# Performance work log

Hardware: AMD Instinct MI355X
Metric: run time of the kernel (lower is better)

The kernel has to match this reference:

```python
import jax, jax.numpy as jnp
import numpy as np

Ng, Np, T, B = 2048, 512, 100, 256


def setup_inputs() -> dict:
    key = jax.random.key(0)
    ks = jax.random.split(key, 16)
    s = lambda fan_in: 1.0 / np.sqrt(fan_in)
    return {
        "v": jax.random.normal(ks[0], (B, T, 2), jnp.float32),
        "p0": jax.random.uniform(ks[1], (B, Np), jnp.float32),
        "enc1_W": jax.random.normal(ks[2], (Np, Ng), jnp.float32) * s(Np),
        "enc1_b": jnp.zeros((Ng,), jnp.float32),
        "enc2_W": jax.random.normal(ks[3], (Np, Ng), jnp.float32) * s(Np),
        "enc2_b": jnp.zeros((Ng,), jnp.float32),
        "M_W": jax.random.normal(ks[4], (2, Ng), jnp.float32) * s(2),
        "M_b": jnp.zeros((Ng,), jnp.float32),
        "lstm_W": jax.random.normal(ks[5], (Ng, 4 * Ng), jnp.float32) * s(Ng),
        "lstm_U": jax.random.normal(ks[6], (Ng, 4 * Ng), jnp.float32) * s(Ng),
        "lstm_b": jnp.zeros((4 * Ng,), jnp.float32),
        "dense_W": jax.random.normal(ks[7], (Ng, Ng), jnp.float32) * s(Ng),
        "dense_b": jnp.zeros((Ng,), jnp.float32),
        "dec_W": jax.random.normal(ks[8], (Ng, Np), jnp.float32) * s(Ng),
        "dec_b": jnp.zeros((Np,), jnp.float32),
    }


def reference(v, p0, enc1_W, enc1_b, enc2_W, enc2_b, M_W, M_b,
              lstm_W, lstm_U, lstm_b, dense_W, dense_b, dec_W, dec_b):
    # initial LSTM state from place-cell code: (h0, c0)
    h0 = p0 @ enc1_W + enc1_b                      # [B, Ng]
    c0 = p0 @ enc2_W + enc2_b                      # [B, Ng]
    Mv = v @ M_W + M_b                             # [B, T, Ng]
    # precompute input-to-gate projections for all timesteps
    x_gates = Mv @ lstm_W + lstm_b                 # [B, T, 4*Ng]

    def step(carry, xt):
        h, c = carry
        z = xt + h @ lstm_U                        # [B, 4*Ng]
        i, f, g, o = jnp.split(z, 4, axis=-1)      # Keras gate order i,f,c,o
        i = jax.nn.sigmoid(i)
        f = jax.nn.sigmoid(f)
        g = jax.nn.relu(g)                         # activation='relu'
        o = jax.nn.sigmoid(o)
        c = f * c + i * g
        h = o * jax.nn.relu(c)
        return (h, c), h

    xs = jnp.swapaxes(x_gates, 0, 1)               # [T, B, 4*Ng]
    _, hs = jax.lax.scan(step, (h0, c0), xs)       # hs: [T, B, Ng]
    rnn = jnp.swapaxes(hs, 0, 1)                   # [B, T, Ng]
    g_cells = jax.nn.relu(rnn @ dense_W + dense_b) # [B, T, Ng]
    place_preds = g_cells @ dec_W + dec_b          # [B, T, Np]
    return place_preds
```

## Files before the change

### kernel.cpp

```cpp
#include <hip/hip_runtime.h>
#include <stdint.h>

#define DI __device__ __forceinline__

typedef short s16x8 __attribute__((ext_vector_type(8)));
typedef float f32x4 __attribute__((ext_vector_type(4)));

#define NG   2048
#define NP   512
#define TT   100
#define BB   256
#define N4   8192
#define MR   25600
#define NBLK 256

DI unsigned short f32_to_bf16(float f) {
  union { float f; uint32_t u; } x; x.f = f;
  uint32_t r = x.u + 0x7fffu + ((x.u >> 16) & 1u);
  return (unsigned short)(r >> 16);
}

DI void async16(const void* g, void* l) {
  __builtin_amdgcn_global_load_lds((const __attribute__((address_space(1))) void*)g,
                                   (__attribute__((address_space(3))) void*)l,
                                   16, 0, 0);
}

DI f32x4 mfma16(s16x8 a, s16x8 b, f32x4 c) {
  return __builtin_amdgcn_mfma_f32_16x16x32_bf16(a, b, c, 0, 0, 0);
}

__global__ __launch_bounds__(256) void k_zero(unsigned* p) {
  if (threadIdx.x < 160) p[threadIdx.x] = 0u;
}

DI void grid_barrier2(unsigned* bar, int xcd, int t) {
  asm volatile("s_waitcnt vmcnt(0)" ::: "memory");
  __syncthreads();
  if (threadIdx.x == 0) {
    unsigned a = __hip_atomic_fetch_add(bar + xcd * 16, 1u,
                                        __ATOMIC_RELAXED, __HIP_MEMORY_SCOPE_AGENT);
    if (a + 1u == 32u * (unsigned)(t + 1)) {
      unsigned g2 = __hip_atomic_fetch_add(bar + 128, 1u,
                                           __ATOMIC_RELAXED, __HIP_MEMORY_SCOPE_AGENT);
      if (g2 + 1u == 8u * (unsigned)(t + 1))
        __hip_atomic_store(bar + 144, (unsigned)(t + 1),
                           __ATOMIC_RELAXED, __HIP_MEMORY_SCOPE_AGENT);
    }
    while (__hip_atomic_load(bar + 144, __ATOMIC_RELAXED,
                             __HIP_MEMORY_SCOPE_AGENT) < (unsigned)(t + 1))
      __builtin_amdgcn_s_sleep(8);
  }
  __syncthreads();
}

template <int BM>
DI void gemm_core_p(const unsigned short* __restrict__ A, int lda, int m0,
                    const unsigned short* __restrict__ Bt, int ldb, int n0, int K,
                    unsigned short* sA, unsigned short* sB, f32x4* acc) {
  constexpr int FM = BM / 32;
  const int tid  = threadIdx.x;
  const int wave = tid >> 6;
  const int lane = tid & 63;
  const int quad = lane >> 4;
  const int lr   = lane & 15;
  const int wm   = wave >> 2;
  const int wn   = wave & 3;
  const int lr8  = lane >> 3;
  const int lc8  = lane & 7;
  const int scol = (lc8 ^ lr8) << 3;

  const int nkt = K >> 6;
  int buf = 0;

  auto stage = [&](int bsel, int k0) {
    unsigned short* dA = sA + bsel * (BM * 64);
    unsigned short* dB = sB + bsel * (128 * 64);
#pragma unroll
    for (int c = 0; c < BM / 64; ++c) {
      int rbase = wave * (BM / 8) + c * 8;
      const unsigned short* g = A + (size_t)(m0 + rbase + lr8) * lda + (k0 + scol);
      async16(g, dA + rbase * 64);
    }
#pragma unroll
    for (int c = 0; c < 2; ++c) {
      int rbase = wave * 16 + c * 8;
      const unsigned short* g = Bt + (size_t)(n0 + rbase + lr8) * ldb + (k0 + scol);
      async16(g, dB + rbase * 64);
    }
  };

  stage(0, 0);
  __syncthreads();
  for (int kt = 0; kt < nkt; ++kt) {
    if (kt + 1 < nkt) stage(buf ^ 1, (kt + 1) << 6);
    const char* cA = (const char*)(sA + buf * (BM * 64));
    const char* cB = (const char*)(sB + buf * (128 * 64));
#pragma unroll
    for (int ks = 0; ks < 2; ++ks) {
      s16x8 af[FM], bfr[2];
#pragma unroll
      for (int fm = 0; fm < FM; ++fm) {
        int row = wm * (BM / 2) + fm * 16 + lr;
        int off = row * 128 + ((ks * 64 + quad * 16) ^ ((row & 7) << 4));
        af[fm] = *(const s16x8*)(cA + off);
      }
#pragma unroll
      for (int fn = 0; fn < 2; ++fn) {
        int col = wn * 32 + fn * 16 + lr;
        int off = col * 128 + ((ks * 64 + quad * 16) ^ ((col & 7) << 4));
        bfr[fn] = *(const s16x8*)(cB + off);
      }
#pragma unroll
      for (int fm = 0; fm < FM; ++fm)
#pragma unroll
        for (int fn = 0; fn < 2; ++fn)
          acc[fm * 2 + fn] = mfma16(af[fm], bfr[fn], acc[fm * 2 + fn]);
    }
    __syncthreads();
    buf ^= 1;
  }
}

template <int MODE>
__global__ __launch_bounds__(256) void k_transpose_bf16(
    const float* __restrict__ src, unsigned short* __restrict__ dst,
    int R, int C, int noff) {
  __shared__ unsigned short tile[64][65];
  int tr0 = blockIdx.x * 64;
  int tc0 = blockIdx.y * 64;
  int tid = threadIdx.x;
#pragma unroll
  for (int i = 0; i < 16; ++i) {
    int idx = tid + i * 256;
    int r = idx >> 6, c = idx & 63;
    tile[r][c] = f32_to_bf16(src[(size_t)(tr0 + r) * C + (tc0 + c)]);
  }
  __syncthreads();
#pragma unroll
  for (int i = 0; i < 16; ++i) {
    int idx = tid + i * 256;
    int cc = idx >> 6, r = idx & 63;
    int c = tc0 + cc;
    int n = (MODE == 0) ? (c + noff) : (((c & 2047) << 2) | (c >> 11));
    dst[(size_t)n * R + (tr0 + r)] = tile[r][cc];
  }
}

__global__ __launch_bounds__(256) void k_cvt(const float* __restrict__ src,
                                             unsigned short* __restrict__ dst, int n) {
  int i = blockIdx.x * 256 + threadIdx.x;
  if (i < n) dst[i] = f32_to_bf16(src[i]);
}

__global__ __launch_bounds__(256) void k_prep_xw_part(
    const float* __restrict__ lstm_W, const float* __restrict__ M_W,
    const float* __restrict__ M_b, float* __restrict__ part) {
  int c = blockIdx.x * 256 + threadIdx.x;
  int kc = blockIdx.y;
  int k0 = kc * 128;
  float a0 = 0.f, a1 = 0.f, ab = 0.f;
  for (int k = k0; k < k0 + 128; ++k) {
    float w = lstm_W[(size_t)k * N4 + c];
    a0 += M_W[k] * w;
    a1 += M_W[NG + k] * w;
    ab += M_b[k] * w;
  }
  float* p = part + (size_t)kc * 3 * N4;
  p[c] = a0; p[N4 + c] = a1; p[2 * N4 + c] = ab;
}

__global__ __launch_bounds__(256) void k_prep_xw_reduce(
    const float* __restrict__ part, const float* __restrict__ lstm_b,
    float* __restrict__ W2r, float* __restrict__ b2r) {
  int c = blockIdx.x * 256 + threadIdx.x;
  float a0 = 0.f, a1 = 0.f, ab = 0.f;
  for (int kc = 0; kc < 16; ++kc) {
    const float* p = part + (size_t)kc * 3 * N4;
    a0 += p[c]; a1 += p[N4 + c]; ab += p[2 * N4 + c];
  }
  int n = ((c & 2047) << 2) | (c >> 11);
  W2r[n] = a0; W2r[N4 + n] = a1; b2r[n] = ab + lstm_b[c];
}

__global__ __launch_bounds__(512) void k_enc(
    const unsigned short* __restrict__ p0b, const unsigned short* __restrict__ encWt,
    const float* __restrict__ enc1_b, const float* __restrict__ enc2_b,
    unsigned short* __restrict__ hbf, float* __restrict__ cfp) {
  __shared__ __align__(16) unsigned short sA[2 * 64 * 64];
  __shared__ __align__(16) unsigned short sB[2 * 128 * 64];
  int m0 = blockIdx.x * 64, n0 = blockIdx.y * 128;
  const f32x4 vzero = {0.f, 0.f, 0.f, 0.f};
  f32x4 acc[4];
#pragma unroll
  for (int i = 0; i < 4; ++i) acc[i] = vzero;
  gemm_core_p<64>(p0b, NP, m0, encWt, NP, n0, NP, sA, sB, acc);

  const int tid = threadIdx.x, wave = tid >> 6, lane = tid & 63;
  const int quad = lane >> 4, lr = lane & 15, wm = wave >> 2, wn = wave & 3;
#pragma unroll
  for (int fm = 0; fm < 2; ++fm)
#pragma unroll
    for (int fn = 0; fn < 2; ++fn)
#pragma unroll
      for (int reg = 0; reg < 4; ++reg) {
        int grow = m0 + wm * 32 + fm * 16 + quad * 4 + reg;
        int gcol = n0 + wn * 32 + fn * 16 + lr;
        float val = acc[fm * 2 + fn][reg];
        if (gcol < NG)
          hbf[(size_t)grow * NG + gcol] = f32_to_bf16(val + enc1_b[gcol]);
        else
          cfp[(size_t)grow * NG + (gcol - NG)] = val + enc2_b[gcol - NG];
      }
}

__global__ __launch_bounds__(512) void k_steps(
    const unsigned short* __restrict__ Ut,
    const float* __restrict__ vv, const float* __restrict__ W2r,
    const float* __restrict__ b2r, float* __restrict__ cfp,
    const unsigned short* __restrict__ hb0,
    unsigned short* __restrict__ hs, unsigned* __restrict__ bar) {
  __shared__ __align__(16) char smem[98304];

  const int bid = blockIdx.x;
  const int xcd = bid & 7, sb = bid >> 3;
  const int mt = sb >> 3, nsub = sb & 7;
  const int nt = xcd * 8 + nsub;
  const int m0 = mt * 64, n0 = nt * 128;
  const int tid = threadIdx.x;
  const int wave = tid >> 6, lane = tid & 63;
  const int quad = lane >> 4, lr = lane & 15, wm = wave >> 2, wn = wave & 3;
  const int lr8 = lane >> 3, lc8 = lane & 7;
  const int scol = (lc8 ^ lr8) << 3;

  const int j = tid & 31;
  const int gbase = n0 + 4 * j;
  const float4 w2a   = *(const float4*)(W2r + gbase);
  const float4 w2b   = *(const float4*)(W2r + N4 + gbase);
  const float4 bbias = *(const float4*)(b2r + gbase);
  const int cell = (n0 >> 2) + j;
  const int r0 = tid >> 5;

  asm volatile("s_waitcnt vmcnt(0)" ::: "memory");

  for (int t = 0; t < TT; ++t) {
    const unsigned short* hin = (t == 0) ? hb0 : (hs + (size_t)(t - 1) * BB * NG);

    const f32x4 vzero = {0.f, 0.f, 0.f, 0.f};
    f32x4 acc[4];
#pragma unroll
    for (int i = 0; i < 4; ++i) acc[i] = vzero;

    auto stageS = [&](int kt) {
      const int slot = kt & 3;
      const int k0 = kt << 6;
      {
        const int rbase = wave * 8;
        const unsigned short* g = hin + (size_t)(m0 + rbase + lr8) * NG + (k0 + scol);
        async16(g, smem + slot * 8192 + rbase * 128);
      }
#pragma unroll
      for (int c = 0; c < 2; ++c) {
        const int rbase = wave * 16 + c * 8;
        const unsigned short* g = Ut + (size_t)(n0 + rbase + lr8) * NG + (k0 + scol);
        async16(g, smem + 32768 + slot * 16384 + rbase * 128);
      }
    };
    auto computeS = [&](int kt) {
      const char* cA = smem + (kt & 3) * 8192;
      const char* cB = smem + 32768 + (kt & 3) * 16384;
#pragma unroll
      for (int ks = 0; ks < 2; ++ks) {
        s16x8 af[2], bfr[2];
#pragma unroll
        for (int fm = 0; fm < 2; ++fm) {
          const int row = wm * 32 + fm * 16 + lr;
          af[fm] = *(const s16x8*)(cA + row * 128 + ((ks * 64 + quad * 16) ^ ((row & 7) << 4)));
        }
#pragma unroll
        for (int fn = 0; fn < 2; ++fn) {
          const int col = wn * 32 + fn * 16 + lr;
          bfr[fn] = *(const s16x8*)(cB + col * 128 + ((ks * 64 + quad * 16) ^ ((col & 7) << 4)));
        }
#pragma unroll
        for (int fm = 0; fm < 2; ++fm)
#pragma unroll
          for (int fn = 0; fn < 2; ++fn)
            acc[fm * 2 + fn] = mfma16(af[fm], bfr[fn], acc[fm * 2 + fn]);
      }
    };

    stageS(0); stageS(1); stageS(2);
    for (int kt = 0; kt < 29; ++kt) {
      asm volatile("s_barrier" ::: "memory");
      stageS(kt + 3);
      asm volatile("s_waitcnt vmcnt(9)\n\ts_barrier" ::: "memory");
      computeS(kt);
    }
    asm volatile("s_waitcnt vmcnt(6)\n\ts_barrier" ::: "memory");
    computeS(29);
    asm volatile("s_waitcnt vmcnt(3)\n\ts_barrier" ::: "memory");
    computeS(30);
    asm volatile("s_waitcnt vmcnt(0)\n\ts_barrier" ::: "memory");
    computeS(31);
    __syncthreads();

    float* zs = (float*)smem;
#pragma unroll
    for (int fm = 0; fm < 2; ++fm)
#pragma unroll
      for (int fn = 0; fn < 2; ++fn)
#pragma unroll
        for (int reg = 0; reg < 4; ++reg) {
          const int r  = wm * 32 + fm * 16 + quad * 4 + reg;
          const int cc = wn * 32 + fn * 16 + lr;
          zs[r * 132 + cc] = acc[fm * 2 + fn][reg];
        }
    __syncthreads();
    unsigned short* htmp = (unsigned short*)(smem + 33792);
#pragma unroll
    for (int i = 0; i < 4; ++i) {
      const int r = r0 + i * 16;
      const int b = m0 + r;
      const float2 vb = *(const float2*)(vv + ((size_t)b * TT + t) * 2);
      float4 z4 = *(const float4*)(zs + r * 132 + 4 * j);
      float zi = z4.x + vb.x * w2a.x + vb.y * w2b.x + bbias.x;
      float zf = z4.y + vb.x * w2a.y + vb.y * w2b.y + bbias.y;
      float zg = z4.z + vb.x * w2a.z + vb.y * w2b.z + bbias.z;
      float zo = z4.w + vb.x * w2a.w + vb.y * w2b.w + bbias.w;
      float i_ = 1.f / (1.f + __expf(-zi));
      float f_ = 1.f / (1.f + __expf(-zf));
      float g_ = fmaxf(zg, 0.f);
      float o_ = 1.f / (1.f + __expf(-zo));
      const size_t ci = (size_t)b * NG + cell;
      float cn = f_ * cfp[ci] + i_ * g_;
      cfp[ci] = cn;
      htmp[r * 32 + j] = f32_to_bf16(o_ * fmaxf(cn, 0.f));
    }
    __syncthreads();
    const unsigned* hw = (const unsigned*)htmp;
#pragma unroll
    for (int p = 0; p < 2; ++p) {
      const int q = tid + p * 512;
      const int r = q >> 4, cq = q & 15;
      unsigned* hp = (unsigned*)(hs + ((size_t)t * BB + m0 + r) * NG + (n0 >> 2)) + cq;
      __hip_atomic_store(hp, hw[q], __ATOMIC_RELAXED, __HIP_MEMORY_SCOPE_AGENT);
    }
    if (t + 1 < TT) grid_barrier2(bar, xcd, t);
  }
}

__global__ __launch_bounds__(512) void k_dense(
    const unsigned short* __restrict__ hs, const unsigned short* __restrict__ dWt,
    const float* __restrict__ dense_b, unsigned short* __restrict__ gc) {
  __shared__ __align__(16) unsigned short sA[2 * 128 * 64];
  __shared__ __align__(16) unsigned short sB[2 * 128 * 64];
  int bid = blockIdx.x;
  int mt = bid >> 4;
  int r4 = bid & 15;
  int nt = ((r4 & 7) << 1) | (r4 >> 3);
  int m0 = mt * 128, n0 = nt * 128;
  const f32x4 vzero = {0.f, 0.f, 0.f, 0.f};
  f32x4 acc[8];
#pragma unroll
  for (int i = 0; i < 8; ++i) acc[i] = vzero;
  gemm_core_p<128>(hs, NG, m0, dWt, NG, n0, NG, sA, sB, acc);

  const int tid = threadIdx.x, wave = tid >> 6, lane = tid & 63;
  const int quad = lane >> 4, lr = lane & 15, wm = wave >> 2, wn = wave & 3;
#pragma unroll
  for (int fm = 0; fm < 4; ++fm)
#pragma unroll
    for (int fn = 0; fn < 2; ++fn)
#pragma unroll
      for (int reg = 0; reg < 4; ++reg) {
        int grow = m0 + wm * 64 + fm * 16 + quad * 4 + reg;
        int gcol = n0 + wn * 32 + fn * 16 + lr;
        float val = fmaxf(acc[fm * 2 + fn][reg] + dense_b[gcol], 0.f);
        gc[(size_t)grow * NG + gcol] = f32_to_bf16(val);
      }
}

__global__ __launch_bounds__(512) void k_dec(
    const unsigned short* __restrict__ gc, const unsigned short* __restrict__ decWt,
    const float* __restrict__ dec_b, float* __restrict__ out) {
  __shared__ __align__(16) unsigned short sA[2 * 128 * 64];
  __shared__ __align__(16) unsigned short sB[2 * 128 * 64];
  int m0 = blockIdx.x * 128, n0 = blockIdx.y * 128;
  const f32x4 vzero = {0.f, 0.f, 0.f, 0.f};
  f32x4 acc[8];
#pragma unroll
  for (int i = 0; i < 8; ++i) acc[i] = vzero;
  gemm_core_p<128>(gc, NG, m0, decWt, NG, n0, NG, sA, sB, acc);

  const int tid = threadIdx.x, wave = tid >> 6, lane = tid & 63;
  const int quad = lane >> 4, lr = lane & 15, wm = wave >> 2, wn = wave & 3;
#pragma unroll
  for (int fm = 0; fm < 4; ++fm)
#pragma unroll
    for (int fn = 0; fn < 2; ++fn)
#pragma unroll
      for (int reg = 0; reg < 4; ++reg) {
        int grow = m0 + wm * 64 + fm * 16 + quad * 4 + reg;
        int gcol = n0 + wn * 32 + fn * 16 + lr;
        int tt = grow >> 8, b = grow & 255;
        out[((size_t)b * TT + tt) * NP + gcol] = acc[fm * 2 + fn][reg] + dec_b[gcol];
      }
}

extern "C" void kernel_launch(void* const* d_in, const int* in_sizes, int n_in,
                              void* d_out, int out_size, void* d_ws, size_t ws_size,
                              hipStream_t stream) {
  (void)in_sizes; (void)n_in; (void)out_size; (void)ws_size;
  const float* v       = (const float*)d_in[0];
  const float* p0      = (const float*)d_in[1];
  const float* enc1_W  = (const float*)d_in[2];
  const float* enc1_b  = (const float*)d_in[3];
  const float* enc2_W  = (const float*)d_in[4];
  const float* enc2_b  = (const float*)d_in[5];
  const float* M_W     = (const float*)d_in[6];
  const float* M_b     = (const float*)d_in[7];
  const float* lstm_W  = (const float*)d_in[8];
  const float* lstm_U  = (const float*)d_in[9];
  const float* lstm_b  = (const float*)d_in[10];
  const float* dense_W = (const float*)d_in[11];
  const float* dense_b = (const float*)d_in[12];
  const float* dec_W   = (const float*)d_in[13];
  const float* dec_b   = (const float*)d_in[14];
  float* out = (float*)d_out;

  char* ws = (char*)d_ws;
  size_t off = 0;
  auto alloc = [&](size_t bytes) {
    char* p = ws + off;
    off += (bytes + 255) & ~(size_t)255;
    return p;
  };
  unsigned short* Ut    = (unsigned short*)alloc((size_t)N4 * NG * 2);
  unsigned short* dWt   = (unsigned short*)alloc((size_t)NG * NG * 2);
  unsigned short* decWt = (unsigned short*)alloc((size_t)NP * NG * 2);
  unsigned short* encWt = (unsigned short*)alloc((size_t)2 * NG * NP * 2);
  unsigned short* p0b   = (unsigned short*)alloc((size_t)BB * NP * 2);
  float* W2r  = (float*)alloc((size_t)2 * N4 * 4);
  float* b2r  = (float*)alloc((size_t)N4 * 4);
  float* part = (float*)alloc((size_t)16 * 3 * N4 * 4);
  float* cfp  = (float*)alloc((size_t)BB * NG * 4);
  unsigned short* hb0 = (unsigned short*)alloc((size_t)BB * NG * 2);
  unsigned short* hs  = (unsigned short*)alloc((size_t)MR * NG * 2);
  unsigned short* gc  = (unsigned short*)alloc((size_t)MR * NG * 2);
  unsigned* bar = (unsigned*)alloc(1024);

  dim3 blk(256), blk5(512);
  k_zero<<<dim3(1), blk, 0, stream>>>(bar);
  k_transpose_bf16<1><<<dim3(32, 128), blk, 0, stream>>>(lstm_U, Ut, NG, N4, 0);
  k_transpose_bf16<0><<<dim3(32, 32), blk, 0, stream>>>(dense_W, dWt, NG, NG, 0);
  k_transpose_bf16<0><<<dim3(32, 8), blk, 0, stream>>>(dec_W, decWt, NG, NP, 0);
  k_transpose_bf16<0><<<dim3(8, 32), blk, 0, stream>>>(enc1_W, encWt, NP, NG, 0);
  k_transpose_bf16<0><<<dim3(8, 32), blk, 0, stream>>>(enc2_W, encWt, NP, NG, NG);
  k_cvt<<<dim3(512), blk, 0, stream>>>(p0, p0b, BB * NP);
  k_prep_xw_part<<<dim3(32, 16), blk, 0, stream>>>(lstm_W, M_W, M_b, part);
  k_prep_xw_reduce<<<dim3(32), blk, 0, stream>>>(part, lstm_b, W2r, b2r);
  k_enc<<<dim3(4, 32), blk5, 0, stream>>>(p0b, encWt, enc1_b, enc2_b, hb0, cfp);
  k_steps<<<dim3(NBLK), blk5, 0, stream>>>(Ut, v, W2r, b2r, cfp, hb0, hs, bar);
  k_dense<<<dim3(3200), blk5, 0, stream>>>(hs, dWt, dense_b, gc);
  k_dec<<<dim3(200, 4), blk5, 0, stream>>>(gc, decWt, dec_b, out);
}
```

Before: 2.135 ms.

## Restructure LSTM step kernel: register-resident cell state, gate-grouped layout, cross-step pipeline

The persistent recurrent kernel now uses 256 threads per block, each wave computing a 32x64 tile. The U-transpose and bias/weight permutations are rearranged so that the i/f/g/o gates for one cell fall in the same lane across four accumulator fragments, which lets the gate math run straight from MFMA accumulators without going through a shared-memory staging tile. Cell state stays in registers for all timesteps instead of being read and written in global memory each step. A 5-slot ring buffer prefetches the first U tiles of the next timestep before the grid barrier, and v values are loaded asynchronously into LDS. The cost is heavier register pressure and more complex wait-count bookkeeping.

Result: faster. 2.091 ms (-2.0%).

```diff
diff --git a/kernel.cpp b/kernel.cpp
--- a/kernel.cpp
+++ b/kernel.cpp
@@ -24,6 +24,11 @@
   __builtin_amdgcn_global_load_lds((const __attribute__((address_space(1))) void*)g,
                                    (__attribute__((address_space(3))) void*)l,
                                    16, 0, 0);
+}
+DI void async4(const void* g, void* l) {
+  __builtin_amdgcn_global_load_lds((const __attribute__((address_space(1))) void*)g,
+                                   (__attribute__((address_space(3))) void*)l,
+                                   4, 0, 0);
 }
 
 DI f32x4 mfma16(s16x8 a, s16x8 b, f32x4 c) {
@@ -142,7 +147,8 @@
     int idx = tid + i * 256;
     int cc = idx >> 6, r = idx & 63;
     int c = tc0 + cc;
-    int n = (MODE == 0) ? (c + noff) : (((c & 2047) << 2) | (c >> 11));
+    int n = (MODE == 0) ? (c + noff)
+                        : ((((c & 2047) >> 4) << 6) | (((c >> 11) & 3) << 4) | (c & 15));
     dst[(size_t)n * R + (tr0 + r)] = tile[r][cc];
   }
 }
@@ -179,7 +185,7 @@
     const float* p = part + (size_t)kc * 3 * N4;
     a0 += p[c]; a1 += p[N4 + c]; ab += p[2 * N4 + c];
   }
-  int n = ((c & 2047) << 2) | (c >> 11);
+  int n = (((c & 2047) >> 4) << 6) | (((c >> 11) & 3) << 4) | (c & 15);
   W2r[n] = a0; W2r[N4 + n] = a1; b2r[n] = ab + lstm_b[c];
 }
 
@@ -214,13 +220,13 @@
       }
 }
 
-__global__ __launch_bounds__(512) void k_steps(
+__global__ __launch_bounds__(256) void k_steps(
     const unsigned short* __restrict__ Ut,
     const float* __restrict__ vv, const float* __restrict__ W2r,
-    const float* __restrict__ b2r, float* __restrict__ cfp,
+    const float* __restrict__ b2r, const float* __restrict__ cfp,
     const unsigned short* __restrict__ hb0,
     unsigned short* __restrict__ hs, unsigned* __restrict__ bar) {
-  __shared__ __align__(16) char smem[98304];
+  __shared__ __align__(16) char smem[127488];
 
   const int bid = blockIdx.x;
   const int xcd = bid & 7, sb = bid >> 3;
@@ -229,125 +235,149 @@
   const int m0 = mt * 64, n0 = nt * 128;
   const int tid = threadIdx.x;
   const int wave = tid >> 6, lane = tid & 63;
-  const int quad = lane >> 4, lr = lane & 15, wm = wave >> 2, wn = wave & 3;
+  const int quad = lane >> 4, lr = lane & 15;
+  const int wm = wave >> 1, wn = wave & 1;
   const int lr8 = lane >> 3, lc8 = lane & 7;
   const int scol = (lc8 ^ lr8) << 3;
 
-  const int j = tid & 31;
-  const int gbase = n0 + 4 * j;
-  const float4 w2a   = *(const float4*)(W2r + gbase);
-  const float4 w2b   = *(const float4*)(W2r + N4 + gbase);
-  const float4 bbias = *(const float4*)(b2r + gbase);
-  const int cell = (n0 >> 2) + j;
-  const int r0 = tid >> 5;
+  float w2x[4], w2y[4], bz[4];
+#pragma unroll
+  for (int g = 0; g < 4; ++g) {
+    const int idx = n0 + wn * 64 + g * 16 + lr;
+    w2x[g] = W2r[idx]; w2y[g] = W2r[N4 + idx]; bz[g] = b2r[idx];
+    asm volatile("" : "+v"(w2x[g])); asm volatile("" : "+v"(w2y[g]));
+    asm volatile("" : "+v"(bz[g]));
+  }
+  const int cellg = nt * 32 + wn * 16 + lr;
+  float cst[2][4];
+#pragma unroll
+  for (int fm = 0; fm < 2; ++fm)
+#pragma unroll
+    for (int reg = 0; reg < 4; ++reg) {
+      const int r = wm * 32 + fm * 16 + quad * 4 + reg;
+      cst[fm][reg] = cfp[(size_t)(m0 + r) * NG + cellg];
+      asm volatile("" : "+v"(cst[fm][reg]));
+    }
+
+  auto stageA = [&](int slot, int kt, const unsigned short* hin) {
+#pragma unroll
+    for (int c = 0; c < 2; ++c) {
+      const int rb = wave * 16 + c * 8;
+      const unsigned short* g = hin + (size_t)(m0 + rb + lr8) * NG + ((kt << 6) + scol);
+      async16(g, smem + slot * 8192 + rb * 128);
+    }
+  };
+  auto stageB = [&](int slot, int k) {
+#pragma unroll
+    for (int c = 0; c < 4; ++c) {
+      const int rb = wave * 32 + c * 8;
+      const unsigned short* g = Ut + (size_t)(n0 + rb + lr8) * NG + (k + scol);
+      async16(g, smem + 40960 + slot * 16384 + rb * 128);
+    }
+  };
+  auto stageV = [&](int t) {
+    const float* gx = vv + ((size_t)(m0 + lane) * TT + t) * 2;
+    async4(gx, smem + 122880);
+    async4(gx + 1, smem + 123136);
+  };
+
+  f32x4 acc[8];
+  auto computeS = [&](int slot) {
+    const char* cA = smem + slot * 8192;
+    const char* cB = smem + 40960 + slot * 16384;
+#pragma unroll
+    for (int ks = 0; ks < 2; ++ks) {
+      s16x8 af[2], bfr[4];
+#pragma unroll
+      for (int fm = 0; fm < 2; ++fm) {
+        const int row = wm * 32 + fm * 16 + lr;
+        af[fm] = *(const s16x8*)(cA + row * 128 + ((ks * 64 + quad * 16) ^ ((row & 7) << 4)));
+      }
+#pragma unroll
+      for (int fn = 0; fn < 4; ++fn) {
+        const int col = wn * 64 + fn * 16 + lr;
+        bfr[fn] = *(const s16x8*)(cB + col * 128 + ((ks * 64 + quad * 16) ^ ((col & 7) << 4)));
+      }
+#pragma unroll
+      for (int fm = 0; fm < 2; ++fm)
+#pragma unroll
+        for (int fn = 0; fn < 4; ++fn)
+          acc[fm * 4 + fn] = mfma16(af[fm], bfr[fn], acc[fm * 4 + fn]);
+    }
+  };
+
+#define INC5(x) x = ((x) == 4) ? 0 : ((x) + 1)
+#define PHASE(W)  asm volatile("s_waitcnt vmcnt(" #W ")\n\ts_barrier" ::: "memory"); \
+                  computeS(cs); INC5(cs);
 
   asm volatile("s_waitcnt vmcnt(0)" ::: "memory");
+  int cs = 0;
+  stageB(0, 0); stageB(1, 64); stageB(2, 128);
 
   for (int t = 0; t < TT; ++t) {
-    const unsigned short* hin = (t == 0) ? hb0 : (hs + (size_t)(t - 1) * BB * NG);
-
+    const unsigned short* hin = t ? hs + (size_t)(t - 1) * BB * NG : hb0;
+    {
+      int s1 = cs; stageA(s1, 0, hin); INC5(s1);
+      stageA(s1, 1, hin); INC5(s1);
+      stageA(s1, 2, hin);
+    }
+    stageV(t);
     const f32x4 vzero = {0.f, 0.f, 0.f, 0.f};
-    f32x4 acc[4];
-#pragma unroll
-    for (int i = 0; i < 4; ++i) acc[i] = vzero;
-
-    auto stageS = [&](int kt) {
-      const int slot = kt & 3;
-      const int k0 = kt << 6;
-      {
-        const int rbase = wave * 8;
-        const unsigned short* g = hin + (size_t)(m0 + rbase + lr8) * NG + (k0 + scol);
-        async16(g, smem + slot * 8192 + rbase * 128);
-      }
-#pragma unroll
-      for (int c = 0; c < 2; ++c) {
-        const int rbase = wave * 16 + c * 8;
-        const unsigned short* g = Ut + (size_t)(n0 + rbase + lr8) * NG + (k0 + scol);
-        async16(g, smem + 32768 + slot * 16384 + rbase * 128);
-      }
-    };
-    auto computeS = [&](int kt) {
-      const char* cA = smem + (kt & 3) * 8192;
-      const char* cB = smem + 32768 + (kt & 3) * 16384;
-#pragma unroll
-      for (int ks = 0; ks < 2; ++ks) {
-        s16x8 af[2], bfr[2];
-#pragma unroll
-        for (int fm = 0; fm < 2; ++fm) {
-          const int row = wm * 32 + fm * 16 + lr;
-          af[fm] = *(const s16x8*)(cA + row * 128 + ((ks * 64 + quad * 16) ^ ((row & 7) << 4)));
-        }
-#pragma unroll
-        for (int fn = 0; fn < 2; ++fn) {
-          const int col = wn * 32 + fn * 16 + lr;
-          bfr[fn] = *(const s16x8*)(cB + col * 128 + ((ks * 64 + quad * 16) ^ ((col & 7) << 4)));
-        }
-#pragma unroll
-        for (int fm = 0; fm < 2; ++fm)
-#pragma unroll
-          for (int fn = 0; fn < 2; ++fn)
-            acc[fm * 2 + fn] = mfma16(af[fm], bfr[fn], acc[fm * 2 + fn]);
-      }
-    };
-
-    stageS(0); stageS(1); stageS(2);
-    for (int kt = 0; kt < 29; ++kt) {
-      asm volatile("s_barrier" ::: "memory");
-      stageS(kt + 3);
-      asm volatile("s_waitcnt vmcnt(9)\n\ts_barrier" ::: "memory");
-      computeS(kt);
-    }
-    asm volatile("s_waitcnt vmcnt(6)\n\ts_barrier" ::: "memory");
-    computeS(29);
-    asm volatile("s_waitcnt vmcnt(3)\n\ts_barrier" ::: "memory");
-    computeS(30);
-    asm volatile("s_waitcnt vmcnt(0)\n\ts_barrier" ::: "memory");
-    computeS(31);
-    __syncthreads();
-
-    float* zs = (float*)smem;
+#pragma unroll
+    for (int i = 0; i < 8; ++i) acc[i] = vzero;
+
+    int ss = cs; INC5(ss); INC5(ss); INC5(ss);
+    stageB(ss, 3 << 6); stageA(ss, 3, hin); INC5(ss);
+    PHASE(12)
+    stageB(ss, 4 << 6); stageA(ss, 4, hin); INC5(ss);
+    PHASE(16)
+    stageB(ss, 5 << 6); stageA(ss, 5, hin); INC5(ss);
+    PHASE(20)
+    for (int p = 3; p <= 28; ++p) {
+      stageB(ss, (p + 3) << 6); stageA(ss, p + 3, hin); INC5(ss);
+      PHASE(18)
+    }
+    stageB(ss, 0); INC5(ss);
+    PHASE(16)
+    stageB(ss, 64); INC5(ss);
+    PHASE(14)
+    stageB(ss, 128); INC5(ss);
+    PHASE(12)
+
+    const float* vx = (const float*)(smem + 122880);
+    const float* vy = (const float*)(smem + 123136);
+    unsigned short* htmp = (unsigned short*)(smem + 123392);
 #pragma unroll
     for (int fm = 0; fm < 2; ++fm)
 #pragma unroll
-      for (int fn = 0; fn < 2; ++fn)
-#pragma unroll
-        for (int reg = 0; reg < 4; ++reg) {
-          const int r  = wm * 32 + fm * 16 + quad * 4 + reg;
-          const int cc = wn * 32 + fn * 16 + lr;
-          zs[r * 132 + cc] = acc[fm * 2 + fn][reg];
-        }
-    __syncthreads();
-    unsigned short* htmp = (unsigned short*)(smem + 33792);
-#pragma unroll
-    for (int i = 0; i < 4; ++i) {
-      const int r = r0 + i * 16;
-      const int b = m0 + r;
-      const float2 vb = *(const float2*)(vv + ((size_t)b * TT + t) * 2);
-      float4 z4 = *(const float4*)(zs + r * 132 + 4 * j);
-      float zi = z4.x + vb.x * w2a.x + vb.y * w2b.x + bbias.x;
-      float zf = z4.y + vb.x * w2a.y + vb.y * w2b.y + bbias.y;
-      float zg = z4.z + vb.x * w2a.z + vb.y * w2b.z + bbias.z;
-      float zo = z4.w + vb.x * w2a.w + vb.y * w2b.w + bbias.w;
-      float i_ = 1.f / (1.f + __expf(-zi));
-      float f_ = 1.f / (1.f + __expf(-zf));
-      float g_ = fmaxf(zg, 0.f);
-      float o_ = 1.f / (1.f + __expf(-zo));
-      const size_t ci = (size_t)b * NG + cell;
-      float cn = f_ * cfp[ci] + i_ * g_;
-      cfp[ci] = cn;
-      htmp[r * 32 + j] = f32_to_bf16(o_ * fmaxf(cn, 0.f));
-    }
+      for (int reg = 0; reg < 4; ++reg) {
+        const int r = wm * 32 + fm * 16 + quad * 4 + reg;
+        const float ax = vx[r], ay = vy[r];
+        float zi = acc[fm * 4 + 0][reg] + ax * w2x[0] + ay * w2y[0] + bz[0];
+        float zf = acc[fm * 4 + 1][reg] + ax * w2x[1] + ay * w2y[1] + bz[1];
+        float zg = acc[fm * 4 + 2][reg] + ax * w2x[2] + ay * w2y[2] + bz[2];
+        float zo = acc[fm * 4 + 3][reg] + ax * w2x[3] + ay * w2y[3] + bz[3];
+        float i_ = 1.f / (1.f + __expf(-zi));
+        float f_ = 1.f / (1.f + __expf(-zf));
+        float g_ = fmaxf(zg, 0.f);
+        float o_ = 1.f / (1.f + __expf(-zo));
+        float cn = f_ * cst[fm][reg] + i_ * g_;
+        cst[fm][reg] = cn;
+        htmp[r * 32 + wn * 16 + lr] = f32_to_bf16(o_ * fmaxf(cn, 0.f));
+      }
     __syncthreads();
     const unsigned* hw = (const unsigned*)htmp;
 #pragma unroll
-    for (int p = 0; p < 2; ++p) {
-      const int q = tid + p * 512;
+    for (int p = 0; p < 4; ++p) {
+      const int q = tid + p * 256;
       const int r = q >> 4, cq = q & 15;
-      unsigned* hp = (unsigned*)(hs + ((size_t)t * BB + m0 + r) * NG + (n0 >> 2)) + cq;
+      unsigned* hp = (unsigned*)(hs + ((size_t)t * BB + m0 + r) * NG) + (nt * 16 + cq);
       __hip_atomic_store(hp, hw[q], __ATOMIC_RELAXED, __HIP_MEMORY_SCOPE_AGENT);
     }
     if (t + 1 < TT) grid_barrier2(bar, xcd, t);
   }
+#undef PHASE
+#undef INC5
 }
 
 __global__ __launch_bounds__(512) void k_dense(
@@ -461,7 +491,7 @@
   k_prep_xw_part<<<dim3(32, 16), blk, 0, stream>>>(lstm_W, M_W, M_b, part);
   k_prep_xw_reduce<<<dim3(32), blk, 0, stream>>>(part, lstm_b, W2r, b2r);
   k_enc<<<dim3(4, 32), blk5, 0, stream>>>(p0b, encWt, enc1_b, enc2_b, hb0, cfp);
-  k_steps<<<dim3(NBLK), blk5, 0, stream>>>(Ut, v, W2r, b2r, cfp, hb0, hs, bar);
+  k_steps<<<dim3(NBLK), blk, 0, stream>>>(Ut, v, W2r, b2r, cfp, hb0, hs, bar);
   k_dense<<<dim3(3200), blk5, 0, stream>>>(hs, dWt, dense_b, gc);
   k_dec<<<dim3(200, 4), blk5, 0, stream>>>(gc, decWt, dec_b, out);
 }
```
